# Optimization experiments

Hardware: AMD Instinct MI355X
Metric: run time of the kernel (lower is better)

The kernel has to match this reference:

```python
import jax, jax.numpy as jnp
import numpy as np

NCLASSES = 21
CONF_THRESH = 0.5
IOU_THRESH = 0.45
TOP_K = 200
NMS_MAX_OUT = 400
NEG = jnp.float32(-1e9)  # sentinel for suppressed / below-threshold scores

B, N_BOXES = 8, 8732
LAST = NCLASSES + 4 * (NCLASSES - 1) + 1  # 102


def setup_inputs() -> dict:
    key = jax.random.key(0)
    kc, kxy, kwh, ke = jax.random.split(key, 4)
    conf = jax.random.uniform(kc, (B, N_BOXES, NCLASSES), dtype=jnp.float32)
    # plausible normalized boxes: xmin,ymin in [0,0.8], width/height in [0.01,0.2]
    xy = jax.random.uniform(kxy, (B, N_BOXES, NCLASSES - 1, 2), minval=0.0, maxval=0.8)
    wh = jax.random.uniform(kwh, (B, N_BOXES, NCLASSES - 1, 2), minval=0.01, maxval=0.2)
    boxes = jnp.concatenate([xy, xy + wh], axis=-1).reshape(B, N_BOXES, 4 * (NCLASSES - 1))
    extra = jax.random.uniform(ke, (B, N_BOXES, 1), dtype=jnp.float32)
    y_pred = jnp.concatenate([conf, boxes, extra], axis=-1)  # [B, N, 102]
    return {"y_pred": y_pred}


def _iou_one_vs_all(box, boxes):
    # box: [4] (xmin,ymin,xmax,ymax); boxes: [N,4]
    x1 = jnp.maximum(box[0], boxes[:, 0])
    y1 = jnp.maximum(box[1], boxes[:, 1])
    x2 = jnp.minimum(box[2], boxes[:, 2])
    y2 = jnp.minimum(box[3], boxes[:, 3])
    inter = jnp.maximum(x2 - x1, 0.0) * jnp.maximum(y2 - y1, 0.0)
    area_a = (box[2] - box[0]) * (box[3] - box[1])
    area_b = (boxes[:, 2] - boxes[:, 0]) * (boxes[:, 3] - boxes[:, 1])
    union = area_a + area_b - inter
    return jnp.where(union > 0.0, inter / union, 0.0)


def _nms_one_class(rows):
    # rows: [N, 7] = (class_id, conf, xmin, ymin, xmax, ymax, extra)
    n = rows.shape[0]
    scores0 = jnp.where(rows[:, 1] > CONF_THRESH, rows[:, 1], NEG)
    boxes = rows[:, 2:6]
    idx_range = jnp.arange(n)

    def step(live, _):
        best = jnp.argmax(live)
        valid = live[best] > NEG * 0.5  # any real score passed the threshold
        ious = _iou_one_vs_all(boxes[best], boxes)
        suppress = valid & ((ious > IOU_THRESH) | (idx_range == best))
        live = jnp.where(suppress, NEG, live)
        return live, (best, valid)

    _, (sel, selv) = jax.lax.scan(step, scores0, None, length=NMS_MAX_OUT)
    # gather selected rows; zero-pad invalid slots (matches tf.pad with 0)
    out = jnp.where(selv[:, None], rows[sel], 0.0)  # [NMS_MAX_OUT, 7]
    return out


def _per_image(item):
    # item: [N, 102]
    n = item.shape[0]
    conf = item[:, 1:NCLASSES]                                  # [N, C-1]
    boxes = item[:, NCLASSES:NCLASSES + 4 * (NCLASSES - 1)].reshape(n, NCLASSES - 1, 4)
    extra = item[:, -1]                                         # [N]
    class_ids = jnp.arange(1, NCLASSES, dtype=item.dtype)       # [C-1]
    rows = jnp.concatenate([
        jnp.broadcast_to(class_ids[:, None, None], (NCLASSES - 1, n, 1)),
        conf.T[:, :, None],
        jnp.transpose(boxes, (1, 0, 2)),
        jnp.broadcast_to(extra[None, :, None], (NCLASSES - 1, n, 1)),
    ], axis=-1)                                                 # [C-1, N, 7]
    per_class = jax.vmap(_nms_one_class)(rows)                  # [C-1, MAX_OUT, 7]
    filtered = per_class.reshape(-1, 7)                         # [(C-1)*MAX_OUT, 7]
    _, top_idx = jax.lax.top_k(filtered[:, 1], TOP_K)           # sorted descending
    return filtered[top_idx]                                    # [TOP_K, 7]


def reference(y_pred):
    return jax.vmap(_per_image)(y_pred)  # [B, TOP_K, 7]
```

## Files before the change

kernel.cpp:

```cpp
#include <hip/hip_runtime.h>
#include <cstdint>

#define NB 8
#define NBOX 8732
#define NCL 21
#define NCM1 20
#define LASTD 102
#define CONF_TH 0.5f
#define IOU_TH 0.45f
#define TOPK 200
#define MAXOUT 400
#define SELCAP 200
#define EMITN 256
#define NTASK (NB * NCM1)
#define THREADS 1024
#define NW 16
#define NIT 9
#define NBIN 2048
#define KPAD 8768
#define NBATCH (KPAD / 64)
#define CPAD 8736

#define MIDD ((double)IOU_TH + 0x1p-26)

struct SM {
    float4 selbox[SELCAP];
    float selA[SELCAP];
    uint64_t selkey[SELCAP];
    uint64_t keys[KPAD];
    uint64_t smask[2][64];
    unsigned long long supW[2][NW];
    int hist[NBIN];
    int binstart[NBIN];
    int wavetot[NW];
    int Mshare, nselshare, prevNshare, doneflag;
};

__device__ __forceinline__ int iou_sup(float4 a, float aA, float4 b, float bA) {
    float x1 = fmaxf(a.x, b.x), y1 = fmaxf(a.y, b.y);
    float x2 = fminf(a.z, b.z), y2 = fminf(a.w, b.w);
    float iw = fmaxf(__fsub_rn(x2, x1), 0.0f);
    float ih = fmaxf(__fsub_rn(y2, y1), 0.0f);
    float inter = __fmul_rn(iw, ih);
    float uni = __fsub_rn(__fadd_rn(aA, bA), inter);
    return (double)inter > MIDD * (double)uni;
}

__device__ __forceinline__ float4 load_box(const float* __restrict__ img,
                                           int boxoff, uint64_t key) {
    if ((key >> 32) == 0) return make_float4(0.f, 0.f, 0.f, 0.f);
    uint32_t i = 0xFFFFFFFFu - (uint32_t)key;
    const float* bp = img + (size_t)i * LASTD + boxoff;
    return make_float4(bp[0], bp[1], bp[2], bp[3]);
}

__device__ __forceinline__ float box_area(float4 b) {
    return __fmul_rn(__fsub_rn(b.z, b.x), __fsub_rn(b.w, b.y));
}

__device__ __forceinline__ float4 shfl_box(float4 b, int c) {
    float4 r;
    r.x = __shfl(b.x, c); r.y = __shfl(b.y, c);
    r.z = __shfl(b.z, c); r.w = __shfl(b.w, c);
    return r;
}

__global__ __launch_bounds__(256) void transpose_conf(const float* __restrict__ yp,
                                                      float* __restrict__ confT,
                                                      float* __restrict__ extraT) {
    const uint32_t TOT4 = (uint32_t)NB * NBOX * LASTD / 4u;
    for (uint32_t i4 = blockIdx.x * blockDim.x + threadIdx.x; i4 < TOT4;
         i4 += gridDim.x * blockDim.x) {
        float4 v = ((const float4*)yp)[i4];
        uint32_t base = i4 * 4u;
        #pragma unroll
        for (int k = 0; k < 4; ++k) {
            uint32_t flat = base + k;
            uint32_t b = flat / (NBOX * LASTD);
            uint32_t rem = flat - b * (NBOX * LASTD);
            uint32_t row = rem / LASTD;
            uint32_t col = rem - row * LASTD;
            float f = (k == 0) ? v.x : (k == 1) ? v.y : (k == 2) ? v.z : v.w;
            if (col - 1u < (uint32_t)NCM1)
                confT[((size_t)b * NCM1 + (col - 1u)) * CPAD + row] = f;
            else if (col == LASTD - 1)
                extraT[(size_t)b * CPAD + row] = f;
        }
    }
}

__device__ void build_keys(const float* __restrict__ confsrc, int cstride,
                           SM& sm, int tid, int lane, int wav) {
    float confs[NIT];
    #pragma unroll
    for (int it = 0; it < NIT; ++it) {
        int idx = it * THREADS + tid;
        confs[it] = (idx < NBOX) ? confsrc[(size_t)idx * cstride] : 0.0f;
    }
    sm.hist[tid] = 0; sm.hist[tid + THREADS] = 0;
    __syncthreads();

    #pragma unroll
    for (int it = 0; it < NIT; ++it) {
        int idx = it * THREADS + tid;
        if (idx < NBOX && confs[it] > CONF_TH) {
            int bin = (int)((__float_as_uint(confs[it]) - 0x3F000000u) >> 12);
            atomicAdd(&sm.hist[bin], 1);
        }
    }
    __syncthreads();

    int h0 = sm.hist[2 * tid], h1 = sm.hist[2 * tid + 1];
    int x = h0 + h1;
    int s = x;
    #pragma unroll
    for (int d = 1; d <= 32; d <<= 1) {
        int y = __shfl_down(s, d);
        if (lane + d < 64) s += y;
    }
    if (lane == 0) sm.wavetot[wav] = s;
    __syncthreads();
    int cross = 0;
    #pragma unroll
    for (int w = 0; w < NW; ++w)
        if (w > wav) cross += sm.wavetot[w];
    int Safter = cross + s - x;
    sm.binstart[2 * tid + 1] = Safter;
    sm.binstart[2 * tid] = Safter + h1;
    if (tid == 0) sm.Mshare = cross + s;
    sm.hist[2 * tid] = 0; sm.hist[2 * tid + 1] = 0;
    __syncthreads();

    #pragma unroll
    for (int it = 0; it < NIT; ++it) {
        int idx = it * THREADS + tid;
        if (idx < NBOX && confs[it] > CONF_TH) {
            uint32_t bits = __float_as_uint(confs[it]);
            int bin = (int)((bits - 0x3F000000u) >> 12);
            int slot = sm.binstart[bin] + atomicAdd(&sm.hist[bin], 1);
            sm.keys[slot] = ((uint64_t)bits << 32) |
                            (uint32_t)(0xFFFFFFFFu - (uint32_t)idx);
        }
    }
    __syncthreads();
    const int M = sm.Mshare;
    for (int m = M + tid; m < KPAD; m += THREADS) sm.keys[m] = 0;
    for (int f = tid; f < NBIN; f += THREADS) {
        int s0 = sm.binstart[f], h = sm.hist[f];
        for (int i2 = 1; i2 < h; ++i2) {
            uint64_t key = sm.keys[s0 + i2];
            int j = i2 - 1;
            while (j >= 0 && sm.keys[s0 + j] < key) {
                sm.keys[s0 + j + 1] = sm.keys[s0 + j];
                --j;
            }
            sm.keys[s0 + j + 1] = key;
        }
    }
    __syncthreads();
}

__device__ int greedy_scan(const float* __restrict__ img, int boxoff, SM& sm,
                           int tid, int lane, int wav) {
    uint64_t keyC = sm.keys[lane];
    uint64_t keyN = sm.keys[64 + lane];
    float4 boxC = load_box(img, boxoff, keyC);
    float4 boxN = load_box(img, boxoff, keyN);
    float aC = box_area(boxC), aN = box_area(boxN);
    #pragma unroll
    for (int tt = 0; tt < 4; ++tt) {
        int c = wav + tt * NW;
        float4 cb = shfl_box(boxC, c);
        float ca = __shfl(aC, c);
        uint64_t row = 0;
        if (ca > 0.0f)
            row = __ballot(lane < c && iou_sup(cb, ca, boxC, aC));
        if (lane == 0) sm.smask[0][c] = row;
    }
    if (tid < 2 * NW) ((unsigned long long*)sm.supW)[tid] = 0ull;
    __syncthreads();

    int nsel = 0, prevN = 0;
    bool done = false;
    for (int i = 0; i < NBATCH && !done; ++i) {
        const int p = i & 1;
        const bool vC = (keyC >> 32) != 0;
        {
            int sup = 0;
            for (int j = prevN + wav; j < nsel; j += NW)
                sup |= iou_sup(boxC, aC, sm.selbox[j], sm.selA[j]);
            unsigned long long bal = __ballot(vC && sup);
            if (lane == 0 && bal) atomicOr(&sm.supW[p][wav], bal);
        }
        int f0 = (i + 2) * 64;
        uint64_t key2 = (f0 < KPAD) ? sm.keys[f0 + lane] : 0;
        float4 box2 = load_box(img, boxoff, key2);
        float a2 = box_area(box2);
        __syncthreads();
        const int nselPre = nsel;
        if (wav == 0) {
            unsigned long long V = __ballot(vC);
            unsigned long long E = (lane < NW) ? sm.supW[p][lane] : 0ull;
            #pragma unroll
            for (int d = 1; d < NW; d <<= 1) E |= __shfl_xor(E, d);
            E = __shfl(E, 0);
            if (lane < NW) sm.supW[p][lane] = 0ull;
            uint64_t smc = sm.smask[p][lane];
            uint64_t alive = ~(E | ~V);
            uint64_t accm = 0;
            int cnt = nsel;
            while (alive && cnt < SELCAP) {
                int t = __ffsll((unsigned long long)alive) - 1;
                uint64_t bit = 1ull << t;
                accm |= bit;
                cnt++;
                unsigned long long kill = __ballot((smc >> t) & 1ull);
                alive &= ~(kill | bit);
            }
            if ((accm >> lane) & 1ull) {
                int pos = nsel + __popcll(accm & ((1ull << lane) - 1ull));
                sm.selbox[pos] = boxC;
                sm.selA[pos] = aC;
                sm.selkey[pos] = keyC;
            }
            if (lane == 0) {
                sm.nselshare = cnt;
                sm.prevNshare = nsel;
                sm.doneflag = (cnt >= SELCAP) || (V != ~0ull);
            }
        } else {
            float4 cb[5];
            float ca[5];
            unsigned amask = 0;
            #pragma unroll
            for (int k = 0; k < 5; ++k) {
                int c = (wav - 1) + k * (NW - 1);
                float4 t4 = make_float4(0.f, 0.f, 0.f, 0.f);
                float tA = 0.0f;
                if (c < 64) {
                    t4 = shfl_box(boxN, c);
                    tA = __shfl(aN, c);
                }
                cb[k] = t4; ca[k] = tA;
                if (c < 64 && tA > 0.0f) amask |= 1u << k;
            }
            unsigned long long sb = 0;
            for (int j0 = 0; j0 < nselPre && amask; j0 += 64) {
                int j = j0 + lane;
                bool jv = j < nselPre;
                float4 sbx = sm.selbox[jv ? j : 0];
                float sA = sm.selA[jv ? j : 0];
                #pragma unroll
                for (int k = 0; k < 5; ++k) {
                    if (!((amask >> k) & 1u)) continue;
                    int hit = jv && iou_sup(cb[k], ca[k], sbx, sA);
                    if (__ballot(hit)) {
                        amask &= ~(1u << k);
                        sb |= 1ull << ((wav - 1) + k * (NW - 1));
                    }
                }
            }
            #pragma unroll
            for (int k = 0; k < 5; ++k) {
                if (!((amask >> k) & 1u)) continue;
                int c = (wav - 1) + k * (NW - 1);
                uint64_t row = __ballot(lane < c && iou_sup(cb[k], ca[k], boxN, aN));
                if (lane == 0) sm.smask[p ^ 1][c] = row;
            }
            if (lane == 0) sm.supW[p ^ 1][wav] = sb;
        }
        __syncthreads();
        nsel = sm.nselshare;
        prevN = sm.prevNshare;
        done = sm.doneflag != 0;
        keyC = keyN; boxC = boxN; aC = aN;
        keyN = key2; boxN = box2; aN = a2;
    }
    return nsel;
}

__device__ void emit_rows(const float* __restrict__ extrasrc, int estride,
                          int cm1, SM& sm, int nsel, float* __restrict__ rows,
                          int task, int tid) {
    float* out0 = rows + (size_t)task * MAXOUT * 7;
    for (int r = tid; r < EMITN; r += THREADS) {
        float* o = out0 + (size_t)r * 7;
        if (r < nsel) {
            uint64_t key = sm.selkey[r];
            uint32_t i = 0xFFFFFFFFu - (uint32_t)key;
            float4 bx = sm.selbox[r];
            o[0] = (float)(cm1 + 1);
            o[1] = __uint_as_float((uint32_t)(key >> 32));
            o[2] = bx.x;
            o[3] = bx.y;
            o[4] = bx.z;
            o[5] = bx.w;
            o[6] = extrasrc[(size_t)i * estride];
        } else {
            #pragma unroll
            for (int q = 0; q < 7; ++q) o[q] = 0.0f;
        }
    }
}

__global__ __launch_bounds__(THREADS) void nms_fast(const float* __restrict__ yp,
                                                    const float* __restrict__ confT,
                                                    const float* __restrict__ extraT,
                                                    float* __restrict__ rows) {
    __shared__ SM sm;
    const int task = blockIdx.x;
    const int b = task / NCM1;
    const int cm1 = task % NCM1;
    const int tid = threadIdx.x;
    const float* img = yp + (size_t)b * NBOX * LASTD;
    build_keys(confT + (size_t)task * CPAD, 1, sm, tid, tid & 63, tid >> 6);
    int nsel = greedy_scan(img, NCL + 4 * cm1, sm, tid, tid & 63, tid >> 6);
    emit_rows(extraT + (size_t)b * CPAD, 1, cm1, sm, nsel, rows, task, tid);
}

__global__ __launch_bounds__(THREADS) void nms_mono(const float* __restrict__ yp,
                                                    float* __restrict__ rows) {
    __shared__ SM sm;
    const int task = blockIdx.x;
    const int b = task / NCM1;
    const int cm1 = task % NCM1;
    const int tid = threadIdx.x;
    const float* img = yp + (size_t)b * NBOX * LASTD;
    build_keys(img + 1 + cm1, LASTD, sm, tid, tid & 63, tid >> 6);
    int nsel = greedy_scan(img, NCL + 4 * cm1, sm, tid, tid & 63, tid >> 6);
    emit_rows(img + (LASTD - 1), LASTD, cm1, sm, nsel, rows, task, tid);
}

__global__ __launch_bounds__(THREADS) void topk_per_image(const float* __restrict__ rows,
                                                          float* __restrict__ out) {
    __shared__ uint64_t K[8192];
    const int b = blockIdx.x;
    const int tid = threadIdx.x;
    const float* rb = rows + (size_t)b * (NCM1 * MAXOUT) * 7;

    for (int xx = tid; xx < 8192; xx += THREADS) {
        int list = xx >> 8, r = xx & 255;
        uint64_t k = 0;
        if (list < NCM1) {
            int flat = list * MAXOUT + r;
            float conf = rb[(size_t)flat * 7 + 1];
            k = ((uint64_t)__float_as_uint(conf) << 32) |
                (uint32_t)(0xFFFFFFFFu - (uint32_t)flat);
        }
        K[xx] = k;
    }
    __syncthreads();

    for (int round = 0; round < 5; ++round) {
        int npairs = 16 >> round;
        int sep = 256 << round;
        for (int w = tid; w < npairs * 256; w += THREADS) {
            int p = w >> 8, t = w & 255;
            int A = p * 2 * sep;
            uint64_t a = K[A + t];
            uint64_t c = K[A + sep + 255 - t];
            K[A + t] = a > c ? a : c;
        }
        __syncthreads();
        for (int j = 128; j >= 1; j >>= 1) {
            for (int w = tid; w < npairs * 128; w += THREADS) {
                int p = w >> 7, q = w & 127;
                int t = ((q & ~(j - 1)) << 1) | (q & (j - 1));
                int A = p * 2 * sep;
                uint64_t x0 = K[A + t];
                uint64_t x1 = K[A + t + j];
                if (x0 < x1) { K[A + t] = x1; K[A + t + j] = x0; }
            }
            __syncthreads();
        }
    }

    if (tid < TOPK) {
        uint64_t key = K[tid];
        uint32_t flat = 0xFFFFFFFFu - (uint32_t)key;
        const float* src = rb + (size_t)flat * 7;
        float* o = out + ((size_t)b * TOPK + tid) * 7;
        #pragma unroll
        for (int q = 0; q < 7; ++q) o[q] = src[q];
    }
}

extern "C" void kernel_launch(void* const* d_in, const int* in_sizes, int n_in,
                              void* d_out, int out_size, void* d_ws, size_t ws_size,
                              hipStream_t stream) {
    const float* yp = (const float*)d_in[0];
    float* rows = (float*)d_ws;
    const size_t rowsB = (size_t)NTASK * MAXOUT * 7 * sizeof(float);
    float* confT = (float*)((char*)d_ws + rowsB);
    const size_t confB = (size_t)NTASK * CPAD * sizeof(float);
    float* extraT = (float*)((char*)confT + confB);
    const size_t extraB = (size_t)NB * CPAD * sizeof(float);
    const size_t need = rowsB + confB + extraB;
    float* out = (float*)d_out;

    if (ws_size >= need) {
        hipLaunchKernelGGL(transpose_conf, dim3(2048), dim3(256), 0, stream,
                           yp, confT, extraT);
        hipLaunchKernelGGL(nms_fast, dim3(NTASK), dim3(THREADS), 0, stream,
                           yp, confT, extraT, rows);
    } else {
        hipLaunchKernelGGL(nms_mono, dim3(NTASK), dim3(THREADS), 0, stream,
                           yp, rows);
    }
    hipLaunchKernelGGL(topk_per_image, dim3(NB), dim3(THREADS), 0, stream,
                       rows, out);
}
```

Before: 66.30 us.

## Fuse per-image top-k into NMS kernel via last-block counter; collapse suppression words

The per-image top-k merge now runs inside the NMS kernel. The last block to finish for each image, detected with a global atomic counter and thread fences, performs the bitonic merge and writes the output. This removes a separate kernel launch and its dependency gap, but adds a memset of the counters. Separately, the per-wave suppression words are replaced by a single shared 64-bit word per parity updated with atomicOr, which drops the cross-lane OR reduction in wave 0.

```diff
diff --git a/kernel.cpp b/kernel.cpp
--- a/kernel.cpp
+++ b/kernel.cpp
@@ -29,7 +29,7 @@
     uint64_t selkey[SELCAP];
     uint64_t keys[KPAD];
     uint64_t smask[2][64];
-    unsigned long long supW[2][NW];
+    unsigned long long extC[2];
     int hist[NBIN];
     int binstart[NBIN];
     int wavetot[NW];
@@ -177,7 +177,7 @@
             row = __ballot(lane < c && iou_sup(cb, ca, boxC, aC));
         if (lane == 0) sm.smask[0][c] = row;
     }
-    if (tid < 2 * NW) ((unsigned long long*)sm.supW)[tid] = 0ull;
+    if (tid == 0) { sm.extC[0] = 0ull; sm.extC[1] = 0ull; }
     __syncthreads();
 
     int nsel = 0, prevN = 0;
@@ -190,7 +190,7 @@
             for (int j = prevN + wav; j < nsel; j += NW)
                 sup |= iou_sup(boxC, aC, sm.selbox[j], sm.selA[j]);
             unsigned long long bal = __ballot(vC && sup);
-            if (lane == 0 && bal) atomicOr(&sm.supW[p][wav], bal);
+            if (lane == 0 && bal) atomicOr(&sm.extC[p], bal);
         }
         int f0 = (i + 2) * 64;
         uint64_t key2 = (f0 < KPAD) ? sm.keys[f0 + lane] : 0;
@@ -200,11 +200,8 @@
         const int nselPre = nsel;
         if (wav == 0) {
             unsigned long long V = __ballot(vC);
-            unsigned long long E = (lane < NW) ? sm.supW[p][lane] : 0ull;
-            #pragma unroll
-            for (int d = 1; d < NW; d <<= 1) E |= __shfl_xor(E, d);
-            E = __shfl(E, 0);
-            if (lane < NW) sm.supW[p][lane] = 0ull;
+            unsigned long long E = sm.extC[p];
+            if (lane == 0) sm.extC[p] = 0ull;
             uint64_t smc = sm.smask[p][lane];
             uint64_t alive = ~(E | ~V);
             uint64_t accm = 0;
@@ -267,7 +264,7 @@
                 uint64_t row = __ballot(lane < c && iou_sup(cb[k], ca[k], boxN, aN));
                 if (lane == 0) sm.smask[p ^ 1][c] = row;
             }
-            if (lane == 0) sm.supW[p ^ 1][wav] = sb;
+            if (lane == 0 && sb) atomicOr(&sm.extC[p ^ 1], sb);
         }
         __syncthreads();
         nsel = sm.nselshare;
@@ -303,11 +300,63 @@
     }
 }
 
-__global__ __launch_bounds__(THREADS) void nms_fast(const float* __restrict__ yp,
+__device__ void topk_merge(uint64_t* K, const float* __restrict__ rb,
+                           float* __restrict__ out, int b, int tid) {
+    for (int xx = tid; xx < 8192; xx += THREADS) {
+        int list = xx >> 8, r = xx & 255;
+        uint64_t k = 0;
+        if (list < NCM1) {
+            int flat = list * MAXOUT + r;
+            float conf = rb[(size_t)flat * 7 + 1];
+            k = ((uint64_t)__float_as_uint(conf) << 32) |
+                (uint32_t)(0xFFFFFFFFu - (uint32_t)flat);
+        }
+        K[xx] = k;
+    }
+    __syncthreads();
+
+    for (int round = 0; round < 5; ++round) {
+        int npairs = 16 >> round;
+        int sep = 256 << round;
+        for (int w = tid; w < npairs * 256; w += THREADS) {
+            int p = w >> 8, t = w & 255;
+            int A = p * 2 * sep;
+            uint64_t a = K[A + t];
+            uint64_t c = K[A + sep + 255 - t];
+            K[A + t] = a > c ? a : c;
+        }
+        __syncthreads();
+        for (int j = 128; j >= 1; j >>= 1) {
+            for (int w = tid; w < npairs * 128; w += THREADS) {
+                int p = w >> 7, q = w & 127;
+                int t = ((q & ~(j - 1)) << 1) | (q & (j - 1));
+                int A = p * 2 * sep;
+                uint64_t x0 = K[A + t];
+                uint64_t x1 = K[A + t + j];
+                if (x0 < x1) { K[A + t] = x1; K[A + t + j] = x0; }
+            }
+            __syncthreads();
+        }
+    }
+
+    if (tid < TOPK) {
+        uint64_t key = K[tid];
+        uint32_t flat = 0xFFFFFFFFu - (uint32_t)key;
+        const float* src = rb + (size_t)flat * 7;
+        float* o = out + ((size_t)b * TOPK + tid) * 7;
+        #pragma unroll
+        for (int q = 0; q < 7; ++q) o[q] = src[q];
+    }
+}
+
+__global__ __launch_bounds__(THREADS) void nms_topk(const float* __restrict__ yp,
                                                     const float* __restrict__ confT,
                                                     const float* __restrict__ extraT,
-                                                    float* __restrict__ rows) {
+                                                    float* __restrict__ rows,
+                                                    int* __restrict__ ctr,
+                                                    float* __restrict__ out) {
     __shared__ SM sm;
+    __shared__ int lastflag;
     const int task = blockIdx.x;
     const int b = task / NCM1;
     const int cm1 = task % NCM1;
@@ -316,6 +365,14 @@
     build_keys(confT + (size_t)task * CPAD, 1, sm, tid, tid & 63, tid >> 6);
     int nsel = greedy_scan(img, NCL + 4 * cm1, sm, tid, tid & 63, tid >> 6);
     emit_rows(extraT + (size_t)b * CPAD, 1, cm1, sm, nsel, rows, task, tid);
+
+    __threadfence();
+    __syncthreads();
+    if (tid == 0) lastflag = (atomicAdd(&ctr[b], 1) == NCM1 - 1);
+    __syncthreads();
+    if (!lastflag) return;
+    __threadfence();
+    topk_merge(sm.keys, rows + (size_t)b * (NCM1 * MAXOUT) * 7, out, b, tid);
 }
 
 __global__ __launch_bounds__(THREADS) void nms_mono(const float* __restrict__ yp,
@@ -335,78 +392,33 @@
                                                           float* __restrict__ out) {
     __shared__ uint64_t K[8192];
     const int b = blockIdx.x;
-    const int tid = threadIdx.x;
-    const float* rb = rows + (size_t)b * (NCM1 * MAXOUT) * 7;
-
-    for (int xx = tid; xx < 8192; xx += THREADS) {
-        int list = xx >> 8, r = xx & 255;
-        uint64_t k = 0;
-        if (list < NCM1) {
-            int flat = list * MAXOUT + r;
-            float conf = rb[(size_t)flat * 7 + 1];
-            k = ((uint64_t)__float_as_uint(conf) << 32) |
-                (uint32_t)(0xFFFFFFFFu - (uint32_t)flat);
-        }
-        K[xx] = k;
-    }
-    __syncthreads();
-
-    for (int round = 0; round < 5; ++round) {
-        int npairs = 16 >> round;
-        int sep = 256 << round;
-        for (int w = tid; w < npairs * 256; w += THREADS) {
-            int p = w >> 8, t = w & 255;
-            int A = p * 2 * sep;
-            uint64_t a = K[A + t];
-            uint64_t c = K[A + sep + 255 - t];
-            K[A + t] = a > c ? a : c;
-        }
-        __syncthreads();
-        for (int j = 128; j >= 1; j >>= 1) {
-            for (int w = tid; w < npairs * 128; w += THREADS) {
-                int p = w >> 7, q = w & 127;
-                int t = ((q & ~(j - 1)) << 1) | (q & (j - 1));
-                int A = p * 2 * sep;
-                uint64_t x0 = K[A + t];
-                uint64_t x1 = K[A + t + j];
-                if (x0 < x1) { K[A + t] = x1; K[A + t + j] = x0; }
-            }
-            __syncthreads();
-        }
-    }
-
-    if (tid < TOPK) {
-        uint64_t key = K[tid];
-        uint32_t flat = 0xFFFFFFFFu - (uint32_t)key;
-        const float* src = rb + (size_t)flat * 7;
-        float* o = out + ((size_t)b * TOPK + tid) * 7;
-        #pragma unroll
-        for (int q = 0; q < 7; ++q) o[q] = src[q];
-    }
+    topk_merge(K, rows + (size_t)b * (NCM1 * MAXOUT) * 7, out, b, threadIdx.x);
 }
 
 extern "C" void kernel_launch(void* const* d_in, const int* in_sizes, int n_in,
                               void* d_out, int out_size, void* d_ws, size_t ws_size,
                               hipStream_t stream) {
     const float* yp = (const float*)d_in[0];
-    float* rows = (float*)d_ws;
+    int* ctr = (int*)d_ws;
+    float* rows = (float*)((char*)d_ws + 256);
     const size_t rowsB = (size_t)NTASK * MAXOUT * 7 * sizeof(float);
-    float* confT = (float*)((char*)d_ws + rowsB);
+    float* confT = (float*)((char*)rows + rowsB);
     const size_t confB = (size_t)NTASK * CPAD * sizeof(float);
     float* extraT = (float*)((char*)confT + confB);
     const size_t extraB = (size_t)NB * CPAD * sizeof(float);
-    const size_t need = rowsB + confB + extraB;
+    const size_t need = 256 + rowsB + confB + extraB;
     float* out = (float*)d_out;
 
     if (ws_size >= need) {
+        hipMemsetAsync(ctr, 0, NB * sizeof(int), stream);
         hipLaunchKernelGGL(transpose_conf, dim3(2048), dim3(256), 0, stream,
                            yp, confT, extraT);
-        hipLaunchKernelGGL(nms_fast, dim3(NTASK), dim3(THREADS), 0, stream,
-                           yp, confT, extraT, rows);
+        hipLaunchKernelGGL(nms_topk, dim3(NTASK), dim3(THREADS), 0, stream,
+                           yp, confT, extraT, rows, ctr, out);
     } else {
         hipLaunchKernelGGL(nms_mono, dim3(NTASK), dim3(THREADS), 0, stream,
                            yp, rows);
-    }
-    hipLaunchKernelGGL(topk_per_image, dim3(NB), dim3(THREADS), 0, stream,
-                       rows, out);
-}
+        hipLaunchKernelGGL(topk_per_image, dim3(NB), dim3(THREADS), 0, stream,
+                           rows, out);
+    }
+}
```

Result: slower. 133.5 us (+101.4%).
